# Kernel tuning notes

Hardware: AMD Instinct MI355X
Metric: run time of the kernel (lower is better)

Reference implementation:

```python
import jax, jax.numpy as jnp
import numpy as np

N = 50000      # nodes
E = 800000     # edges (before self-loops)
F_IN = 128     # input node features
H = 4          # attention heads
C = 32         # hidden channels per head (concat width = H*C = 128)
CLS = 40       # num classes (layer 4, concat=False -> mean over heads)
NEG_SLOPE = 0.2


def setup_inputs() -> dict:
    key = jax.random.key(0)
    ks = jax.random.split(key, 16)
    w = lambda k, shape: (jax.random.normal(k, shape, jnp.float32) * 0.1)
    return {
        "x": jax.random.normal(ks[0], (N, F_IN), jnp.float32),
        "edge_index": jax.random.randint(ks[1], (2, E), 0, N),
        "W1": w(ks[2], (F_IN, H * C)), "att_src1": w(ks[3], (H, C)), "att_dst1": w(ks[4], (H, C)), "b1": jnp.zeros((H * C,), jnp.float32),
        "W2": w(ks[5], (H * C, H * C)), "att_src2": w(ks[6], (H, C)), "att_dst2": w(ks[7], (H, C)), "b2": jnp.zeros((H * C,), jnp.float32),
        "W3": w(ks[8], (H * C, H * C)), "att_src3": w(ks[9], (H, C)), "att_dst3": w(ks[10], (H, C)), "b3": jnp.zeros((H * C,), jnp.float32),
        "W4": w(ks[11], (H * C, H * CLS)), "att_src4": w(ks[12], (H, CLS)), "att_dst4": w(ks[13], (H, CLS)), "b4": jnp.zeros((CLS,), jnp.float32),
    }


def _gat(x, W, a_src, a_dst, b, src, dst, n, heads, ch, concat):
    # Linear transform, per-head view: [n, heads, ch]
    h = (x @ W).reshape(n, heads, ch)
    # per-node scalar attention terms [n, heads]
    es = (h * a_src).sum(-1)
    ed = (h * a_dst).sum(-1)
    # edge logits: alpha_j (source) + alpha_i (target), leaky relu (PyG GATConv)
    e = jax.nn.leaky_relu(es[src] + ed[dst], NEG_SLOPE)  # [Etot, heads]
    # segment softmax over incoming edges of each dst node (self-loops guarantee >=1 edge)
    m = jax.ops.segment_max(e, dst, num_segments=n)
    ealpha = jnp.exp(e - m[dst])
    denom = jax.ops.segment_sum(ealpha, dst, num_segments=n)
    alpha = ealpha / denom[dst]
    # weighted message aggregation (scatter-add)
    out = jax.ops.segment_sum(h[src] * alpha[:, :, None], dst, num_segments=n)
    out = out.reshape(n, heads * ch) if concat else out.mean(axis=1)
    return out + b


def reference(x, edge_index, W1, att_src1, att_dst1, b1, W2, att_src2, att_dst2, b2,
              W3, att_src3, att_dst3, b3, W4, att_src4, att_dst4, b4):
    n = x.shape[0]
    loop = jnp.arange(n)
    src = jnp.concatenate([edge_index[0], loop])  # add self-loops (PyG default)
    dst = jnp.concatenate([edge_index[1], loop])
    # dropout layers are identity in eval mode (training=False)
    h = _gat(x, W1, att_src1, att_dst1, b1, src, dst, n, H, C, True)
    h = jax.nn.relu(h)
    h = _gat(h, W2, att_src2, att_dst2, b2, src, dst, n, H, C, True)
    h = jax.nn.relu(h)
    h = _gat(h, W3, att_src3, att_dst3, b3, src, dst, n, H, C, True)
    h = jax.nn.relu(h)
    h = _gat(h, W4, att_src4, att_dst4, b4, src, dst, n, H, CLS, False)
    return h
```

## Files before the change

### kernel.cpp

```cpp
#include <hip/hip_runtime.h>
#include <math.h>

#define NN 50000
#define EE 800000
#define ET (EE + NN)
#define NCHK ((NN + 255) / 256)
#define NEG 0.2f

__device__ __forceinline__ float lrelu(float x) { return x > 0.f ? x : NEG * x; }

typedef __bf16 bf16x8 __attribute__((ext_vector_type(8)));
typedef float f32x4 __attribute__((ext_vector_type(4)));


__global__ __launch_bounds__(256) void k_init_cnt(int* cnt) {
    int i = blockIdx.x * 256 + threadIdx.x;
    if (i < NN) cnt[i] = 1;
}

__global__ __launch_bounds__(256) void k_hist(const int* __restrict__ eidx, int* __restrict__ cnt) {
    int i = blockIdx.x * 256 + threadIdx.x;
    if (i < EE) atomicAdd(&cnt[eidx[EE + i]], 1);
}

__global__ __launch_bounds__(256) void k_csum(const int* __restrict__ cnt, int* __restrict__ csums) {
    __shared__ int sh[256];
    int t = threadIdx.x, i = blockIdx.x * 256 + t;
    sh[t] = (i < NN) ? cnt[i] : 0;
    __syncthreads();
    for (int off = 128; off > 0; off >>= 1) {
        if (t < off) sh[t] += sh[t + off];
        __syncthreads();
    }
    if (t == 0) csums[blockIdx.x] = sh[0];
}

__global__ __launch_bounds__(256) void k_cscan(int* __restrict__ csums, int* __restrict__ rowptr) {
    __shared__ int sh[256];
    int t = threadIdx.x;
    sh[t] = (t < NCHK) ? csums[t] : 0;
    __syncthreads();
    for (int off = 1; off < 256; off <<= 1) {
        int x = (t >= off) ? sh[t - off] : 0;
        __syncthreads();
        sh[t] += x;
        __syncthreads();
    }
    int ex = (t == 0) ? 0 : sh[t - 1];
    if (t < NCHK) csums[t] = ex;
    if (t == 0) rowptr[NN] = ET;
}

__global__ __launch_bounds__(256) void k_chscan(const int* __restrict__ cnt, const int* __restrict__ csums,
                                                int* __restrict__ rowptr, int* __restrict__ cursor) {
    __shared__ int sh[256];
    int t = threadIdx.x, b = blockIdx.x, i = b * 256 + t;
    int v = (i < NN) ? cnt[i] : 0;
    sh[t] = v;
    __syncthreads();
    for (int off = 1; off < 256; off <<= 1) {
        int x = (t >= off) ? sh[t - off] : 0;
        __syncthreads();
        sh[t] += x;
        __syncthreads();
    }
    int ex = (t == 0 ? 0 : sh[t - 1]) + csums[b];
    if (i < NN) { rowptr[i] = ex; cursor[i] = ex; }
}

__global__ __launch_bounds__(256) void k_scatter(const int* __restrict__ eidx,
                                                 int* __restrict__ cursor, int* __restrict__ ssrc) {
    int i = blockIdx.x * 256 + threadIdx.x;
    if (i >= ET) return;
    int s, d;
    if (i < EE) { s = eidx[i]; d = eidx[EE + i]; } else { s = d = i - EE; }
    int pos = atomicAdd(&cursor[d], 1);
    ssrc[pos] = s;
}


template <int NOUT>
__global__ __launch_bounds__(256) void k_gemm_mfma(const float* __restrict__ X,
                                                   const float* __restrict__ Wm,
                                                   float* __restrict__ Y) {
    constexpr int NT = NOUT / 16;
    __shared__ __bf16 WH[4][NOUT][8];
    __shared__ __bf16 WL[4][NOUT][8];
    int tid = threadIdx.x;
    int w = tid >> 6, l = tid & 63;
    int rb = blockIdx.x * 64;
    int arow = rb + w * 16 + (l & 15);
    int rclamp = arow < NN ? arow : NN - 1;
    int kg = l >> 4;
    f32x4 acc[NT];
    #pragma unroll
    for (int t = 0; t < NT; ++t) acc[t] = (f32x4){0.f, 0.f, 0.f, 0.f};

    for (int kc = 0; kc < 128; kc += 32) {
        for (int idx = tid; idx < 32 * NOUT; idx += 256) {
            int kk = idx / NOUT;
            int c  = idx - kk * NOUT;
            float v = Wm[(size_t)(kc + kk) * NOUT + c];
            __bf16 hi = (__bf16)v;
            __bf16 lo = (__bf16)(v - (float)hi);
            WH[kk >> 3][c][kk & 7] = hi;
            WL[kk >> 3][c][kk & 7] = lo;
        }
        __syncthreads();

        float4 aA = *reinterpret_cast<const float4*>(&X[(size_t)rclamp * 128 + kc + kg * 8]);
        float4 aB = *reinterpret_cast<const float4*>(&X[(size_t)rclamp * 128 + kc + kg * 8 + 4]);
        float av[8] = {aA.x, aA.y, aA.z, aA.w, aB.x, aB.y, aB.z, aB.w};
        bf16x8 ahi, alo;
        #pragma unroll
        for (int j = 0; j < 8; ++j) {
            __bf16 h = (__bf16)av[j];
            ahi[j] = h;
            alo[j] = (__bf16)(av[j] - (float)h);
        }

        #pragma unroll
        for (int t = 0; t < NT; ++t) {
            bf16x8 bhi = *reinterpret_cast<const bf16x8*>(&WH[kg][t * 16 + (l & 15)][0]);
            bf16x8 blo = *reinterpret_cast<const bf16x8*>(&WL[kg][t * 16 + (l & 15)][0]);
            acc[t] = __builtin_amdgcn_mfma_f32_16x16x32_bf16(ahi, bhi, acc[t], 0, 0, 0);
            acc[t] = __builtin_amdgcn_mfma_f32_16x16x32_bf16(alo, bhi, acc[t], 0, 0, 0);
            acc[t] = __builtin_amdgcn_mfma_f32_16x16x32_bf16(ahi, blo, acc[t], 0, 0, 0);
        }
        __syncthreads();
    }

    #pragma unroll
    for (int t = 0; t < NT; ++t) {
        int cc = t * 16 + (l & 15);
        #pragma unroll
        for (int i = 0; i < 4; ++i) {
            int rr = rb + w * 16 + (l >> 4) * 4 + i;
            if (rr < NN) Y[(size_t)rr * NOUT + cc] = acc[t][i];
        }
    }
}


template <int CH>
__global__ __launch_bounds__(256) void k_attn_scal(const float* __restrict__ Hf,
                                                   const float* __restrict__ asrc,
                                                   const float* __restrict__ adst,
                                                   float* __restrict__ es, float* __restrict__ ed) {
    int i = blockIdx.x * 256 + threadIdx.x;
    if (i >= NN * 4) return;
    int h = i & 3, n = i >> 2;
    const float4* row = reinterpret_cast<const float4*>(Hf + (size_t)n * (4 * CH) + h * CH);
    const float4* As  = reinterpret_cast<const float4*>(asrc + h * CH);
    const float4* Ad  = reinterpret_cast<const float4*>(adst + h * CH);
    float s = 0.f, d = 0.f;
    #pragma unroll
    for (int c = 0; c < CH / 4; ++c) {
        float4 v = row[c], a = As[c], b = Ad[c];
        s += v.x * a.x + v.y * a.y + v.z * a.z + v.w * a.w;
        d += v.x * b.x + v.y * b.y + v.z * b.z + v.w * b.w;
    }
    es[i] = s;
    ed[i] = d;
}


__global__ __launch_bounds__(256) void k_agg128(const float* __restrict__ Hf,
                                                const float* __restrict__ es, const float* __restrict__ ed,
                                                const int* __restrict__ rowptr, const int* __restrict__ ssrc,
                                                const float* __restrict__ bias, float* __restrict__ Yout) {
    int wid = (blockIdx.x * 256 + threadIdx.x) >> 6;
    int lane = threadIdx.x & 63;
    if (wid >= NN) return;
    int n = wid;
    int beg = rowptr[n], end = rowptr[n + 1];
    int h1 = lane & 3;
    int eoff = lane >> 2;
    float edv = ed[n * 4 + h1];

    float m = -1e30f, dsum = 0.f;
    for (int idx = beg + eoff; idx < end; idx += 16) {
        int s = ssrc[idx];
        float e = lrelu(es[s * 4 + h1] + edv);
        float M = fmaxf(m, e);
        dsum = dsum * __expf(m - M) + __expf(e - M);
        m = M;
    }
    #pragma unroll
    for (int off = 4; off < 64; off <<= 1) {
        float om = __shfl_xor(m, off);
        float od = __shfl_xor(dsum, off);
        float M = fmaxf(m, om);
        dsum = dsum * __expf(m - M) + od * __expf(om - M);
        m = M;
    }
    float invd = 1.f / dsum;

    int c = lane * 2;
    int hc = lane >> 4;
    const float* __restrict__ Hc = Hf + c;
    float ax = 0.f, ay = 0.f;
    int base = beg;
    int nfull = (end - beg) >> 4;
    for (int ch = 0; ch < nfull; ++ch, base += 16) {
        int s = ssrc[base + eoff];
        float e = lrelu(es[s * 4 + h1] + edv);
        float alpha = __expf(e - m) * invd;
        #pragma unroll
        for (int e2 = 0; e2 < 16; ++e2) {
            int se = __shfl(s, e2 * 4);
            float p = __shfl(alpha, e2 * 4 + hc);
            float2 v = *reinterpret_cast<const float2*>(&Hc[(size_t)se * 128]);
            ax += p * v.x;
            ay += p * v.y;
        }
    }
    if (base < end) {
        int cnt = end - base;
        int myIdx = base + eoff;
        int s = ssrc[myIdx < end ? myIdx : end - 1];
        float e = lrelu(es[s * 4 + h1] + edv);
        float alpha = (myIdx < end) ? __expf(e - m) * invd : 0.f;
        for (int e2 = 0; e2 < cnt; ++e2) {
            int se = __shfl(s, e2 * 4);
            float p = __shfl(alpha, e2 * 4 + hc);
            float2 v = *reinterpret_cast<const float2*>(&Hc[(size_t)se * 128]);
            ax += p * v.x;
            ay += p * v.y;
        }
    }
    Yout[(size_t)n * 128 + c]     = fmaxf(ax + bias[c], 0.f);
    Yout[(size_t)n * 128 + c + 1] = fmaxf(ay + bias[c + 1], 0.f);
}


__global__ __launch_bounds__(256) void k_agg160_mean(const float* __restrict__ Hf,
                                                     const float* __restrict__ es, const float* __restrict__ ed,
                                                     const int* __restrict__ rowptr, const int* __restrict__ ssrc,
                                                     const float* __restrict__ b4, float* __restrict__ out) {
    int wid = (blockIdx.x * 256 + threadIdx.x) >> 6;
    int lane = threadIdx.x & 63;
    if (wid >= NN) return;
    int n = wid;
    int beg = rowptr[n], end = rowptr[n + 1];
    int h1 = lane & 3;
    int eoff = lane >> 2;
    float edv = ed[n * 4 + h1];

    float m = -1e30f, dsum = 0.f;
    for (int idx = beg + eoff; idx < end; idx += 16) {
        int s = ssrc[idx];
        float e = lrelu(es[s * 4 + h1] + edv);
        float M = fmaxf(m, e);
        dsum = dsum * __expf(m - M) + __expf(e - M);
        m = M;
    }
    #pragma unroll
    for (int off = 4; off < 64; off <<= 1) {
        float om = __shfl_xor(m, off);
        float od = __shfl_xor(dsum, off);
        float M = fmaxf(m, om);
        dsum = dsum * __expf(m - M) + od * __expf(om - M);
        m = M;
    }
    float invd = 1.f / dsum;

    bool act = (lane < 40);
    const float* __restrict__ Hc = Hf + lane;
    float a = 0.f;
    int base = beg;
    int nfull = (end - beg) >> 4;
    for (int ch = 0; ch < nfull; ++ch, base += 16) {
        int s = ssrc[base + eoff];
        float e = lrelu(es[s * 4 + h1] + edv);
        float alpha = __expf(e - m) * invd;
        #pragma unroll
        for (int e2 = 0; e2 < 16; ++e2) {
            int se = __shfl(s, e2 * 4);
            float p0 = __shfl(alpha, e2 * 4 + 0);
            float p1 = __shfl(alpha, e2 * 4 + 1);
            float p2 = __shfl(alpha, e2 * 4 + 2);
            float p3 = __shfl(alpha, e2 * 4 + 3);
            if (act) {
                const float* r = Hc + (size_t)se * 160;
                a += p0 * r[0] + p1 * r[40] + p2 * r[80] + p3 * r[120];
            }
        }
    }
    if (base < end) {
        int cnt = end - base;
        int myIdx = base + eoff;
        int s = ssrc[myIdx < end ? myIdx : end - 1];
        float e = lrelu(es[s * 4 + h1] + edv);
        float alpha = (myIdx < end) ? __expf(e - m) * invd : 0.f;
        for (int e2 = 0; e2 < cnt; ++e2) {
            int se = __shfl(s, e2 * 4);
            float p0 = __shfl(alpha, e2 * 4 + 0);
            float p1 = __shfl(alpha, e2 * 4 + 1);
            float p2 = __shfl(alpha, e2 * 4 + 2);
            float p3 = __shfl(alpha, e2 * 4 + 3);
            if (act) {
                const float* r = Hc + (size_t)se * 160;
                a += p0 * r[0] + p1 * r[40] + p2 * r[80] + p3 * r[120];
            }
        }
    }
    if (act) out[(size_t)n * 40 + lane] = 0.25f * a + b4[lane];
}


extern "C" void kernel_launch(void* const* d_in, const int* in_sizes, int n_in,
                              void* d_out, int out_size, void* d_ws, size_t ws_size,
                              hipStream_t stream) {
    const float* x    = (const float*)d_in[0];
    const int*   eidx = (const int*)d_in[1];
    const float* W[4]    = {(const float*)d_in[2], (const float*)d_in[6], (const float*)d_in[10], (const float*)d_in[14]};
    const float* asrc[4] = {(const float*)d_in[3], (const float*)d_in[7], (const float*)d_in[11], (const float*)d_in[15]};
    const float* adst[4] = {(const float*)d_in[4], (const float*)d_in[8], (const float*)d_in[12], (const float*)d_in[16]};
    const float* bias[4] = {(const float*)d_in[5], (const float*)d_in[9], (const float*)d_in[13], (const float*)d_in[17]};
    float* out = (float*)d_out;

    float* hA = (float*)d_ws;
    float* hB = hA + (size_t)NN * 160;
    float* es = hB + (size_t)NN * 160;
    float* ed = es + (size_t)NN * 4;
    int* rowptr = (int*)(ed + (size_t)NN * 4);
    int* cnt    = rowptr + (NN + 1);
    int* cursor = cnt + NN;
    int* ssrc   = cursor + NN;
    int* csums  = ssrc + ET;

    k_init_cnt<<<(NN + 255) / 256, 256, 0, stream>>>(cnt);
    k_hist<<<(EE + 255) / 256, 256, 0, stream>>>(eidx, cnt);
    k_csum<<<NCHK, 256, 0, stream>>>(cnt, csums);
    k_cscan<<<1, 256, 0, stream>>>(csums, rowptr);
    k_chscan<<<NCHK, 256, 0, stream>>>(cnt, csums, rowptr, cursor);
    k_scatter<<<(ET + 255) / 256, 256, 0, stream>>>(eidx, cursor, ssrc);

    int gemmBlocks = (NN + 63) / 64;
    int aggBlocks = (NN * 64 + 255) / 256;

    k_gemm_mfma<128><<<gemmBlocks, 256, 0, stream>>>(x, W[0], hA);
    k_attn_scal<32><<<(NN * 4 + 255) / 256, 256, 0, stream>>>(hA, asrc[0], adst[0], es, ed);
    k_agg128<<<aggBlocks, 256, 0, stream>>>(hA, es, ed, rowptr, ssrc, bias[0], hB);

    k_gemm_mfma<128><<<gemmBlocks, 256, 0, stream>>>(hB, W[1], hA);
    k_attn_scal<32><<<(NN * 4 + 255) / 256, 256, 0, stream>>>(hA, asrc[1], adst[1], es, ed);
    k_agg128<<<aggBlocks, 256, 0, stream>>>(hA, es, ed, rowptr, ssrc, bias[1], hB);

    k_gemm_mfma<128><<<gemmBlocks, 256, 0, stream>>>(hB, W[2], hA);
    k_attn_scal<32><<<(NN * 4 + 255) / 256, 256, 0, stream>>>(hA, asrc[2], adst[2], es, ed);
    k_agg128<<<aggBlocks, 256, 0, stream>>>(hA, es, ed, rowptr, ssrc, bias[2], hB);

    k_gemm_mfma<160><<<gemmBlocks, 256, 0, stream>>>(hB, W[3], hA);
    k_attn_scal<40><<<(NN * 4 + 255) / 256, 256, 0, stream>>>(hA, asrc[3], adst[3], es, ed);
    k_agg160_mean<<<aggBlocks, 256, 0, stream>>>(hA, es, ed, rowptr, ssrc, bias[3], out);
}
```

Before: 553.7 us.

## Gather 8 edges per wave iteration with float4 row loads and reduce

Both aggregation kernels now split each wave into 8 edge groups of 8 lanes, where each lane loads float4 chunks of a source row. Previously the wave walked edges one at a time with float2 or scalar loads. Partial sums are combined with an xor-shuffle reduction across the edge groups. The 40-class mean kernel stages the reduced row in shared memory to average the heads. This is meant to put more independent gathers in flight and widen memory accesses, at the cost of extra registers and a cross-lane reduction per node.

New measurement: 510.1 us. 1.09x faster.

```diff
diff --git a/kernel.cpp b/kernel.cpp
--- a/kernel.cpp
+++ b/kernel.cpp
@@ -196,41 +196,59 @@
     }
     float invd = 1.f / dsum;
 
-    int c = lane * 2;
-    int hc = lane >> 4;
-    const float* __restrict__ Hc = Hf + c;
-    float ax = 0.f, ay = 0.f;
+    int q = lane & 7;
+    int eg8 = lane >> 3;
+    f32x4 acc4[4];
+    #pragma unroll
+    for (int i = 0; i < 4; ++i) acc4[i] = (f32x4){0.f, 0.f, 0.f, 0.f};
+
+    int nch = (end - beg + 15) >> 4;
     int base = beg;
-    int nfull = (end - beg) >> 4;
-    for (int ch = 0; ch < nfull; ++ch, base += 16) {
-        int s = ssrc[base + eoff];
-        float e = lrelu(es[s * 4 + h1] + edv);
-        float alpha = __expf(e - m) * invd;
-        #pragma unroll
-        for (int e2 = 0; e2 < 16; ++e2) {
-            int se = __shfl(s, e2 * 4);
-            float p = __shfl(alpha, e2 * 4 + hc);
-            float2 v = *reinterpret_cast<const float2*>(&Hc[(size_t)se * 128]);
-            ax += p * v.x;
-            ay += p * v.y;
-        }
-    }
-    if (base < end) {
-        int cnt = end - base;
+    for (int ch = 0; ch < nch; ++ch, base += 16) {
         int myIdx = base + eoff;
         int s = ssrc[myIdx < end ? myIdx : end - 1];
         float e = lrelu(es[s * 4 + h1] + edv);
         float alpha = (myIdx < end) ? __expf(e - m) * invd : 0.f;
-        for (int e2 = 0; e2 < cnt; ++e2) {
-            int se = __shfl(s, e2 * 4);
-            float p = __shfl(alpha, e2 * 4 + hc);
-            float2 v = *reinterpret_cast<const float2*>(&Hc[(size_t)se * 128]);
-            ax += p * v.x;
-            ay += p * v.y;
-        }
-    }
-    Yout[(size_t)n * 128 + c]     = fmaxf(ax + bias[c], 0.f);
-    Yout[(size_t)n * 128 + c + 1] = fmaxf(ay + bias[c + 1], 0.f);
+        #pragma unroll
+        for (int hb = 0; hb < 2; ++hb) {
+            int e16 = hb * 8 + eg8;
+            int se = __shfl(s, e16 * 4);
+            const float* rowp = Hf + (size_t)se * 128 + q * 4;
+            #pragma unroll
+            for (int i = 0; i < 4; ++i) {
+                float p = __shfl(alpha, e16 * 4 + i);
+                float4 v = *reinterpret_cast<const float4*>(rowp + i * 32);
+                acc4[i].x += p * v.x;
+                acc4[i].y += p * v.y;
+                acc4[i].z += p * v.z;
+                acc4[i].w += p * v.w;
+            }
+        }
+    }
+
+    #pragma unroll
+    for (int off = 8; off < 64; off <<= 1) {
+        #pragma unroll
+        for (int i = 0; i < 4; ++i) {
+            acc4[i].x += __shfl_xor(acc4[i].x, off);
+            acc4[i].y += __shfl_xor(acc4[i].y, off);
+            acc4[i].z += __shfl_xor(acc4[i].z, off);
+            acc4[i].w += __shfl_xor(acc4[i].w, off);
+        }
+    }
+    if (lane < 8) {
+        #pragma unroll
+        for (int i = 0; i < 4; ++i) {
+            int c0 = 32 * i + 4 * lane;
+            float4 bv = *reinterpret_cast<const float4*>(&bias[c0]);
+            float4 o;
+            o.x = fmaxf(acc4[i].x + bv.x, 0.f);
+            o.y = fmaxf(acc4[i].y + bv.y, 0.f);
+            o.z = fmaxf(acc4[i].z + bv.z, 0.f);
+            o.w = fmaxf(acc4[i].w + bv.w, 0.f);
+            *reinterpret_cast<float4*>(&Yout[(size_t)n * 128 + c0]) = o;
+        }
+    }
 }
 
 
@@ -238,8 +256,10 @@
                                                      const float* __restrict__ es, const float* __restrict__ ed,
                                                      const int* __restrict__ rowptr, const int* __restrict__ ssrc,
                                                      const float* __restrict__ b4, float* __restrict__ out) {
+    __shared__ float buf[4][160];
     int wid = (blockIdx.x * 256 + threadIdx.x) >> 6;
     int lane = threadIdx.x & 63;
+    int w = threadIdx.x >> 6;
     if (wid >= NN) return;
     int n = wid;
     int beg = rowptr[n], end = rowptr[n + 1];
@@ -265,47 +285,59 @@
     }
     float invd = 1.f / dsum;
 
-    bool act = (lane < 40);
-    const float* __restrict__ Hc = Hf + lane;
-    float a = 0.f;
+    int q = lane & 7;
+    int eg8 = lane >> 3;
+    int hh[5];
+    #pragma unroll
+    for (int i = 0; i < 5; ++i) hh[i] = (i * 8 + q) / 10;
+    f32x4 acc4[5];
+    #pragma unroll
+    for (int i = 0; i < 5; ++i) acc4[i] = (f32x4){0.f, 0.f, 0.f, 0.f};
+
+    int nch = (end - beg + 15) >> 4;
     int base = beg;
-    int nfull = (end - beg) >> 4;
-    for (int ch = 0; ch < nfull; ++ch, base += 16) {
-        int s = ssrc[base + eoff];
-        float e = lrelu(es[s * 4 + h1] + edv);
-        float alpha = __expf(e - m) * invd;
-        #pragma unroll
-        for (int e2 = 0; e2 < 16; ++e2) {
-            int se = __shfl(s, e2 * 4);
-            float p0 = __shfl(alpha, e2 * 4 + 0);
-            float p1 = __shfl(alpha, e2 * 4 + 1);
-            float p2 = __shfl(alpha, e2 * 4 + 2);
-            float p3 = __shfl(alpha, e2 * 4 + 3);
-            if (act) {
-                const float* r = Hc + (size_t)se * 160;
-                a += p0 * r[0] + p1 * r[40] + p2 * r[80] + p3 * r[120];
-            }
-        }
-    }
-    if (base < end) {
-        int cnt = end - base;
+    for (int ch = 0; ch < nch; ++ch, base += 16) {
         int myIdx = base + eoff;
         int s = ssrc[myIdx < end ? myIdx : end - 1];
         float e = lrelu(es[s * 4 + h1] + edv);
         float alpha = (myIdx < end) ? __expf(e - m) * invd : 0.f;
-        for (int e2 = 0; e2 < cnt; ++e2) {
-            int se = __shfl(s, e2 * 4);
-            float p0 = __shfl(alpha, e2 * 4 + 0);
-            float p1 = __shfl(alpha, e2 * 4 + 1);
-            float p2 = __shfl(alpha, e2 * 4 + 2);
-            float p3 = __shfl(alpha, e2 * 4 + 3);
-            if (act) {
-                const float* r = Hc + (size_t)se * 160;
-                a += p0 * r[0] + p1 * r[40] + p2 * r[80] + p3 * r[120];
+        #pragma unroll
+        for (int hb = 0; hb < 2; ++hb) {
+            int e16 = hb * 8 + eg8;
+            int se = __shfl(s, e16 * 4);
+            const float* rowp = Hf + (size_t)se * 160 + q * 4;
+            #pragma unroll
+            for (int i = 0; i < 5; ++i) {
+                float p = __shfl(alpha, e16 * 4 + hh[i]);
+                float4 v = *reinterpret_cast<const float4*>(rowp + i * 32);
+                acc4[i].x += p * v.x;
+                acc4[i].y += p * v.y;
+                acc4[i].z += p * v.z;
+                acc4[i].w += p * v.w;
             }
         }
     }
-    if (act) out[(size_t)n * 40 + lane] = 0.25f * a + b4[lane];
+
+    #pragma unroll
+    for (int off = 8; off < 64; off <<= 1) {
+        #pragma unroll
+        for (int i = 0; i < 5; ++i) {
+            acc4[i].x += __shfl_xor(acc4[i].x, off);
+            acc4[i].y += __shfl_xor(acc4[i].y, off);
+            acc4[i].z += __shfl_xor(acc4[i].z, off);
+            acc4[i].w += __shfl_xor(acc4[i].w, off);
+        }
+    }
+    if (lane < 8) {
+        #pragma unroll
+        for (int i = 0; i < 5; ++i)
+            *reinterpret_cast<float4*>(&buf[w][32 * i + 4 * lane]) = (float4){acc4[i].x, acc4[i].y, acc4[i].z, acc4[i].w};
+    }
+    __builtin_amdgcn_wave_barrier();
+    if (lane < 40) {
+        float v = 0.25f * (buf[w][lane] + buf[w][lane + 40] + buf[w][lane + 80] + buf[w][lane + 120]) + b4[lane];
+        out[(size_t)n * 40 + lane] = v;
+    }
 }
 
 
```
